# Optimization experiments

Hardware: AMD Instinct MI355X
Metric: run time of the kernel (lower is better)

Reference implementation:

```python
import jax, jax.numpy as jnp
import numpy as np

B, M, L, D = 4, 128, 512, 768
NEG = -1e30


def setup_inputs() -> dict:
    key = jax.random.key(0)
    k1, k2 = jax.random.split(key)
    h = jax.random.normal(k1, (B, L, D), dtype=jnp.float32)
    mention_masks = jax.random.randint(k2, (B, M, L), 0, 2, dtype=jnp.int32)
    return {"h": h, "mention_masks": mention_masks}


def reference(h, mention_masks):
    # h: [B, L, D]; mention_masks: [B, M, L] (0/1)
    # Faithful to: m = (mask == 0).float() * -1e30; (m + h).max(dim=2)
    m = (mention_masks == 0).astype(h.dtype) * NEG          # [B, M, L]
    # broadcast add then max over token dim L -> [B, M, D]
    mention_reprs = jnp.max(h[:, None, :, :] + m[:, :, :, None], axis=2)
    return mention_reprs
```

## Files before the change

### kernel.cpp

```cpp
#include <hip/hip_runtime.h>

#define BB 4
#define MM 128
#define LL 512
#define DD 768
#define NEGF (-1e30f)

struct F3 { float x, y, z; };

__global__ __launch_bounds__(1024, 4) void mention_max_kernel(
    const float* __restrict__ h, const int* __restrict__ mask,
    float* __restrict__ out)
{
    const int lane = threadIdx.x & 63;
    const int wave = threadIdx.x >> 6;
    const int dch  = blockIdx.x;
    const int mch  = blockIdx.y;
    const int b    = blockIdx.z;

    const int d0 = dch * 192 + lane * 3;
    const int m0 = mch * 8;
    const int l0 = wave * 32;

    const int half = lane >> 5;
    const int lrow = lane & 31;
    const int* mp = mask + ((size_t)(b * MM + m0)) * LL + l0 + lrow;
    int mv0 = mp[(0 + half) * LL];
    int mv1 = mp[(2 + half) * LL];
    int mv2 = mp[(4 + half) * LL];
    int mv3 = mp[(6 + half) * LL];

    const F3* hp = (const F3*)(h + ((size_t)(b * LL + l0)) * DD + d0);
    F3 ra[24];
#pragma unroll
    for (int i = 0; i < 24; ++i) ra[i] = hp[(size_t)i * (DD / 3)];

    unsigned wbits[8];
    { unsigned long long bl = __ballot(mv0 != 0);
      wbits[0] = __builtin_amdgcn_readfirstlane((unsigned)bl);
      wbits[1] = __builtin_amdgcn_readfirstlane((unsigned)(bl >> 32)); }
    { unsigned long long bl = __ballot(mv1 != 0);
      wbits[2] = __builtin_amdgcn_readfirstlane((unsigned)bl);
      wbits[3] = __builtin_amdgcn_readfirstlane((unsigned)(bl >> 32)); }
    { unsigned long long bl = __ballot(mv2 != 0);
      wbits[4] = __builtin_amdgcn_readfirstlane((unsigned)bl);
      wbits[5] = __builtin_amdgcn_readfirstlane((unsigned)(bl >> 32)); }
    { unsigned long long bl = __ballot(mv3 != 0);
      wbits[6] = __builtin_amdgcn_readfirstlane((unsigned)bl);
      wbits[7] = __builtin_amdgcn_readfirstlane((unsigned)(bl >> 32)); }

    F3 acc[8];
#pragma unroll
    for (int m = 0; m < 8; ++m) { acc[m].x = NEGF; acc[m].y = NEGF; acc[m].z = NEGF; }

#define ROWUPD(R, I)                                                          \
    _Pragma("unroll")                                                         \
    for (int m = 0; m < 8; ++m) {                                             \
        if ((wbits[m] >> (I)) & 1u) {                                         \
            acc[m].x = fmaxf(acc[m].x, (R).x);                                \
            acc[m].y = fmaxf(acc[m].y, (R).y);                                \
            acc[m].z = fmaxf(acc[m].z, (R).z);                                \
        }                                                                     \
    }

#pragma unroll
    for (int i = 0; i < 8; ++i) { ROWUPD(ra[i], i) }

    F3 rb[8];
#pragma unroll
    for (int i = 0; i < 8; ++i) rb[i] = hp[(size_t)(i + 24) * (DD / 3)];

#pragma unroll
    for (int i = 8; i < 24; ++i) { ROWUPD(ra[i], i) }
#pragma unroll
    for (int i = 0; i < 8; ++i) { ROWUPD(rb[i], i + 24) }
#undef ROWUPD

    __shared__ float red[8][8][3][64];
    if (wave >= 8) {
#pragma unroll
        for (int m = 0; m < 8; ++m) {
            red[wave - 8][m][0][lane] = acc[m].x;
            red[wave - 8][m][1][lane] = acc[m].y;
            red[wave - 8][m][2][lane] = acc[m].z;
        }
    }
    __syncthreads();
    if (wave < 8) {
#pragma unroll
        for (int m = 0; m < 8; ++m) {
            red[wave][m][0][lane] = fmaxf(acc[m].x, red[wave][m][0][lane]);
            red[wave][m][1][lane] = fmaxf(acc[m].y, red[wave][m][1][lane]);
            red[wave][m][2][lane] = fmaxf(acc[m].z, red[wave][m][2][lane]);
        }
    }
    __syncthreads();

    if (threadIdx.x < 512) {
        const int m  = (int)(threadIdx.x >> 6);
        const int ln = (int)(threadIdx.x & 63);
        float vx = red[0][m][0][ln];
        float vy = red[0][m][1][ln];
        float vz = red[0][m][2][ln];
#pragma unroll
        for (int w = 1; w < 8; ++w) {
            vx = fmaxf(vx, red[w][m][0][ln]);
            vy = fmaxf(vy, red[w][m][1][ln]);
            vz = fmaxf(vz, red[w][m][2][ln]);
        }
        float* op = out + ((size_t)(b * MM + m0 + m)) * DD + dch * 192 + ln * 3;
        op[0] = vx;
        op[1] = vy;
        op[2] = vz;
    }
}

extern "C" void kernel_launch(void* const* d_in, const int* in_sizes, int n_in,
                              void* d_out, int out_size, void* d_ws, size_t ws_size,
                              hipStream_t stream) {
    const float* h    = (const float*)d_in[0];
    const int*   mask = (const int*)d_in[1];
    float*       out  = (float*)d_out;
    dim3 grid(DD / 192, MM / 8, BB);
    mention_max_kernel<<<grid, dim3(1024), 0, stream>>>(h, mask, out);
}
```

Baseline: 70.43 us.

## Stream h rows through LDS with direct global-to-LDS loads in a ring

Replaces the register-held 32-row F3 loads with a five-slot per-wave LDS ring buffer filled by global_load_lds, with explicit vmcnt waits so loads overlap the max updates. It also switches the per-lane column mapping from strided 3-float groups to coalesced 64-lane stripes, changing the output write pattern to match. This aims to cut register pressure and improve coalescing and overlap. In exchange it adds LDS traffic, hand-placed waitcnt asm whose correctness depends on exact instruction counts, and a larger shared allocation that may limit occupancy.

```diff
diff --git a/kernel.cpp b/kernel.cpp
--- a/kernel.cpp
+++ b/kernel.cpp
@@ -6,7 +6,12 @@
 #define DD 768
 #define NEGF (-1e30f)
 
-struct F3 { float x, y, z; };
+
+typedef __attribute__((address_space(1))) const unsigned int gu32_t;
+typedef __attribute__((address_space(3))) unsigned int lu32_t;
+
+#define WAITVM(N) asm volatile("s_waitcnt vmcnt(" #N ")" ::: "memory")
+#define WAITLGKM0() asm volatile("s_waitcnt lgkmcnt(0)" ::: "memory")
 
 __global__ __launch_bounds__(1024, 4) void mention_max_kernel(
     const float* __restrict__ h, const int* __restrict__ mask,
@@ -18,9 +23,10 @@
     const int mch  = blockIdx.y;
     const int b    = blockIdx.z;
 
-    const int d0 = dch * 192 + lane * 3;
     const int m0 = mch * 8;
     const int l0 = wave * 32;
+
+    __shared__ float smem[15360];
 
     const int half = lane >> 5;
     const int lrow = lane & 31;
@@ -30,10 +36,22 @@
     int mv2 = mp[(4 + half) * LL];
     int mv3 = mp[(6 + half) * LL];
 
-    const F3* hp = (const F3*)(h + ((size_t)(b * LL + l0)) * DD + d0);
-    F3 ra[24];
-#pragma unroll
-    for (int i = 0; i < 24; ++i) ra[i] = hp[(size_t)i * (DD / 3)];
+    const float* growbase = h + ((size_t)(b * LL + l0)) * DD + dch * 192;
+    float* sbase = smem + wave * 960;
+
+#define ISSUE(J) do {                                                         \
+        __builtin_amdgcn_global_load_lds(                                     \
+            (gu32_t*)(growbase + (size_t)(J) * DD + 0 * 64 + lane),           \
+            (lu32_t*)(sbase + ((J) % 5) * 192 + 0 * 64), 4, 0, 0);            \
+        __builtin_amdgcn_global_load_lds(                                     \
+            (gu32_t*)(growbase + (size_t)(J) * DD + 1 * 64 + lane),           \
+            (lu32_t*)(sbase + ((J) % 5) * 192 + 1 * 64), 4, 0, 0);            \
+        __builtin_amdgcn_global_load_lds(                                     \
+            (gu32_t*)(growbase + (size_t)(J) * DD + 2 * 64 + lane),           \
+            (lu32_t*)(sbase + ((J) % 5) * 192 + 2 * 64), 4, 0, 0);            \
+    } while (0)
+
+    ISSUE(0); ISSUE(1); ISSUE(2); ISSUE(3); ISSUE(4);
 
     unsigned wbits[8];
     { unsigned long long bl = __ballot(mv0 != 0);
@@ -49,49 +67,57 @@
       wbits[6] = __builtin_amdgcn_readfirstlane((unsigned)bl);
       wbits[7] = __builtin_amdgcn_readfirstlane((unsigned)(bl >> 32)); }
 
-    F3 acc[8];
+    float accx[8], accy[8], accz[8];
 #pragma unroll
-    for (int m = 0; m < 8; ++m) { acc[m].x = NEGF; acc[m].y = NEGF; acc[m].z = NEGF; }
+    for (int m = 0; m < 8; ++m) { accx[m] = NEGF; accy[m] = NEGF; accz[m] = NEGF; }
 
-#define ROWUPD(R, I)                                                          \
-    _Pragma("unroll")                                                         \
-    for (int m = 0; m < 8; ++m) {                                             \
-        if ((wbits[m] >> (I)) & 1u) {                                         \
-            acc[m].x = fmaxf(acc[m].x, (R).x);                                \
-            acc[m].y = fmaxf(acc[m].y, (R).y);                                \
-            acc[m].z = fmaxf(acc[m].z, (R).z);                                \
+#define CONSUME(I) do {                                                       \
+        const float* sp = sbase + ((I) % 5) * 192;                            \
+        const float vx = sp[lane];                                            \
+        const float vy = sp[64 + lane];                                       \
+        const float vz = sp[128 + lane];                                      \
+        _Pragma("unroll")                                                     \
+        for (int m = 0; m < 8; ++m) {                                         \
+            if ((wbits[m] >> (I)) & 1u) {                                     \
+                accx[m] = fmaxf(accx[m], vx);                                 \
+                accy[m] = fmaxf(accy[m], vy);                                 \
+                accz[m] = fmaxf(accz[m], vz);                                 \
+            }                                                                 \
         }                                                                     \
-    }
+    } while (0)
 
 #pragma unroll
-    for (int i = 0; i < 8; ++i) { ROWUPD(ra[i], i) }
+    for (int i = 0; i < 27; ++i) {
+        WAITVM(12);
+        CONSUME(i);
+        WAITLGKM0();
+        ISSUE(i + 5);
+    }
+    WAITVM(12); CONSUME(27);
+    WAITVM(9);  CONSUME(28);
+    WAITVM(6);  CONSUME(29);
+    WAITVM(3);  CONSUME(30);
+    WAITVM(0);  CONSUME(31);
+#undef CONSUME
+#undef ISSUE
 
-    F3 rb[8];
-#pragma unroll
-    for (int i = 0; i < 8; ++i) rb[i] = hp[(size_t)(i + 24) * (DD / 3)];
-
-#pragma unroll
-    for (int i = 8; i < 24; ++i) { ROWUPD(ra[i], i) }
-#pragma unroll
-    for (int i = 0; i < 8; ++i) { ROWUPD(rb[i], i + 24) }
-#undef ROWUPD
-
-    __shared__ float red[8][8][3][64];
+    __syncthreads();
+    float (*red)[8][3][64] = (float (*)[8][3][64])smem;
     if (wave >= 8) {
 #pragma unroll
         for (int m = 0; m < 8; ++m) {
-            red[wave - 8][m][0][lane] = acc[m].x;
-            red[wave - 8][m][1][lane] = acc[m].y;
-            red[wave - 8][m][2][lane] = acc[m].z;
+            red[wave - 8][m][0][lane] = accx[m];
+            red[wave - 8][m][1][lane] = accy[m];
+            red[wave - 8][m][2][lane] = accz[m];
         }
     }
     __syncthreads();
     if (wave < 8) {
 #pragma unroll
         for (int m = 0; m < 8; ++m) {
-            red[wave][m][0][lane] = fmaxf(acc[m].x, red[wave][m][0][lane]);
-            red[wave][m][1][lane] = fmaxf(acc[m].y, red[wave][m][1][lane]);
-            red[wave][m][2][lane] = fmaxf(acc[m].z, red[wave][m][2][lane]);
+            red[wave][m][0][lane] = fmaxf(accx[m], red[wave][m][0][lane]);
+            red[wave][m][1][lane] = fmaxf(accy[m], red[wave][m][1][lane]);
+            red[wave][m][2][lane] = fmaxf(accz[m], red[wave][m][2][lane]);
         }
     }
     __syncthreads();
@@ -108,10 +134,10 @@
             vy = fmaxf(vy, red[w][m][1][ln]);
             vz = fmaxf(vz, red[w][m][2][ln]);
         }
-        float* op = out + ((size_t)(b * MM + m0 + m)) * DD + dch * 192 + ln * 3;
-        op[0] = vx;
-        op[1] = vy;
-        op[2] = vz;
+        float* op = out + ((size_t)(b * MM + m0 + m)) * DD + dch * 192;
+        op[ln]       = vx;
+        op[64 + ln]  = vy;
+        op[128 + ln] = vz;
     }
 }
 
```

After: 74.21 us. 5.4% more time.
